# Kernel tuning notes

Hardware: AMD Instinct MI355X
Metric: run time of the kernel (lower is better)

The kernel has to match this reference:

```python
import jax, jax.numpy as jnp
import numpy as np

T = 4096
HID = 64          # hidden size (hard-coded 64 in forward)
EMB = 8           # direction embed size
NA = 7            # num actions
CONV_OUT = 64 * 15 * 15   # 64x64 input -> 31x31 -> 15x15, 64 channels
RIN = CONV_OUT + EMB      # GRU input size = 14408


def setup_inputs() -> dict:
    key = jax.random.key(0)
    ks = jax.random.split(key, 16)
    s = 0.05
    return {
        "image": jax.random.uniform(ks[0], (T, 1, 64, 64, 3), dtype=jnp.float32) * 255.0,
        "direction": jax.random.randint(ks[1], (T, 1), 0, 4),
        "conv1_w": jax.random.normal(ks[2], (32, 3, 3, 3), dtype=jnp.float32) * s,
        "conv1_b": jax.random.normal(ks[3], (32,), dtype=jnp.float32) * s,
        "conv2_w": jax.random.normal(ks[4], (64, 32, 3, 3), dtype=jnp.float32) * s,
        "conv2_b": jax.random.normal(ks[5], (64,), dtype=jnp.float32) * s,
        "emb": jax.random.normal(ks[6], (4, EMB), dtype=jnp.float32) * s,
        "w_ih": jax.random.normal(ks[7], (3 * HID, RIN), dtype=jnp.float32) * s,
        "b_ih": jax.random.normal(ks[8], (3 * HID,), dtype=jnp.float32) * s,
        "w_hh": jax.random.normal(ks[9], (3 * HID, HID), dtype=jnp.float32) * s,
        "b_hh": jax.random.normal(ks[10], (3 * HID,), dtype=jnp.float32) * s,
        "actor_w": jax.random.normal(ks[11], (NA, HID), dtype=jnp.float32) * s,
        "actor_b": jax.random.normal(ks[12], (NA,), dtype=jnp.float32) * s,
        "critic_w": jax.random.normal(ks[13], (1, HID), dtype=jnp.float32) * s,
        "critic_b": jax.random.normal(ks[14], (1,), dtype=jnp.float32) * s,
    }


def _conv(x, w, b):
    y = jax.lax.conv_general_dilated(x, w, (2, 2), 'VALID',
                                     dimension_numbers=('NCHW', 'OIHW', 'NCHW'))
    return jax.nn.relu(y + b[None, :, None, None])


def reference(image, direction, conv1_w, conv1_b, conv2_w, conv2_b, emb,
              w_ih, b_ih, w_hh, b_hh, actor_w, actor_b, critic_w, critic_b):
    img = image[:, 0]              # [T,H,W,3]  (squeeze env-batch dim)
    d = direction[:, 0]            # [T]
    x = (img / 255.0).transpose(0, 3, 1, 2)        # NCHW [T,3,64,64]
    x = _conv(x, conv1_w, conv1_b)                 # [T,32,31,31]
    x = _conv(x, conv2_w, conv2_b)                 # [T,64,15,15]
    conv_out = x.reshape(x.shape[0], -1)           # [T,14400] (C,H,W order == torch Flatten)
    feat = jnp.concatenate([conv_out, emb[d]], axis=1)   # [T,RIN]

    # Precompute input-side gate projections for all timesteps in one GEMM
    gx = feat @ w_ih.T + b_ih                      # [T,3H]

    def step(h, gx_t):
        gh = h @ w_hh.T + b_hh                     # [3H]
        r = jax.nn.sigmoid(gx_t[:HID] + gh[:HID])
        z = jax.nn.sigmoid(gx_t[HID:2*HID] + gh[HID:2*HID])
        n = jnp.tanh(gx_t[2*HID:] + r * gh[2*HID:])
        h_new = (1.0 - z) * n + z * h
        return h_new, h_new

    _, hs = jax.lax.scan(step, jnp.zeros((HID,), dtype=feat.dtype), gx)  # [T,HID]

    logits = hs @ actor_w.T + actor_b              # [T,NA]
    values = (hs @ critic_w.T + critic_b)[:, 0]    # [T]
    policy = jax.nn.softmax(logits, axis=-1)
    return policy, values
```

## Files before the change

kernel.cpp:

```cpp
#include <hip/hip_runtime.h>

#define T_STEPS 4096
#define HID 64
#define FEAT_LD 14464
#define SPLITK 8

typedef unsigned int uint;
typedef unsigned short ushort_t;
typedef _Float16 h2v __attribute__((ext_vector_type(2)));
typedef _Float16 v8h __attribute__((ext_vector_type(8)));
typedef float v4f __attribute__((ext_vector_type(4)));

__device__ __forceinline__ uint cvtpk(float a, float b) {
  return __builtin_bit_cast(uint, __builtin_amdgcn_cvt_pkrtz(a, b));
}
__device__ __forceinline__ uint packrelu(float a, float b) {
  return __builtin_bit_cast(
      uint, __builtin_amdgcn_cvt_pkrtz(fmaxf(a, 0.f), fmaxf(b, 0.f)));
}
__device__ __forceinline__ ushort_t hrelu(float a) {
  _Float16 h = (_Float16)fmaxf(a, 0.f);
  return __builtin_bit_cast(ushort_t, h);
}

__global__ __launch_bounds__(256) void prep_b(const float* __restrict__ w_ih,
                                              _Float16* __restrict__ Bw) {
  int i = blockIdx.x * 256 + threadIdx.x;
  if (i >= 192 * FEAT_LD) return;
  int row = i / FEAT_LD, col = i - row * FEAT_LD;
  float v = 0.f;
  if (col < 14400) {
    int p = col >> 6, oc = col & 63;
    v = w_ih[row * 14408 + oc * 225 + p];
  } else if (col < 14408) {
    v = w_ih[row * 14408 + col];
  }
  Bw[i] = (_Float16)v;
}

__global__ __launch_bounds__(256) void prep_conv(const float* __restrict__ w1,
                                                 const float* __restrict__ w2,
                                                 _Float16* __restrict__ bpack1,
                                                 _Float16* __restrict__ bpack) {
  int t = blockIdx.x * 256 + threadIdx.x;
  if (t < 2048) {
    int j = t & 7, l = (t >> 3) & 63, nf = (t >> 9) & 1, ks = t >> 10;
    int k = ks * 32 + ((l >> 4) * 8) + j;
    int cc = k & 3, kk = k >> 2;
    int oc = nf * 16 + (l & 15);
    float v = (cc < 3 && kk < 9) ? w1[oc * 27 + cc * 9 + kk] : 0.f;
    bpack1[t] = (_Float16)v;
  }
  if (t < 18432) {
    int j = t & 7, l = (t >> 3) & 63, nf = (t >> 9) & 3, kk = t >> 11;
    int oc = nf * 16 + (l & 15), ic = (l >> 4) * 8 + j;
    bpack[t] = (_Float16)w2[oc * 288 + ic * 9 + kk];
  }
}

__global__ __launch_bounds__(512, 4) void conv_kernel(
    const float* __restrict__ image, const int* __restrict__ dir,
    const _Float16* __restrict__ bpack1, const float* __restrict__ b1,
    const _Float16* __restrict__ bpack, const float* __restrict__ b2,
    const float* __restrict__ emb, _Float16* __restrict__ feat, int imgBase) {
  __shared__ __align__(16) _Float16 img_s[1216 * 4];
  __shared__ __align__(16) char c1_s[288 * 64];

  ushort_t* out_s = (ushort_t*)img_s;

  const int tid = threadIdx.x;
  const int wid = tid >> 6, lane = tid & 63;
  const int lrow = lane & 15, lq = lane >> 4;
  const int qh = blockIdx.x;
  const int img = imgBase + blockIdx.y;
  const int q3 = (qh == 3);
  const int nrows = q3 ? 16 : 19;
  const int nvalid = q3 ? 217 : 279;
  const int npos = q3 ? 45 : 60;
  const float* ip = image + (size_t)img * 12288 + (size_t)qh * 16 * 192;
  _Float16* fr = feat + (size_t)blockIdx.y * FEAT_LD;

  const int nf = wid & 3, mh = wid >> 2;
  v8h wb[9];
#pragma unroll
  for (int kk = 0; kk < 9; ++kk)
    wb[kk] = *(const v8h*)(bpack + ((size_t)(kk * 4 + nf) * 64 + lane) * 8);

  v8h bw1[2][2];
#pragma unroll
  for (int f = 0; f < 2; ++f)
#pragma unroll
    for (int ks = 0; ks < 2; ++ks)
      bw1[f][ks] =
          *(const v8h*)(bpack1 + ((size_t)(ks * 2 + f) * 64 + lane) * 8);
  const float4 b1q0 = *(const float4*)(b1 + lq * 4);
  const float4 b1q1 = *(const float4*)(b1 + 16 + lq * 4);

  const float kn = 1.f / 255.f;
  const int ng = nrows * 16;
  for (int g = tid; g < ng; g += 512) {
    const float* s0 = ip + g * 12;
    float4 A = *(const float4*)s0, B = *(const float4*)(s0 + 4),
           C = *(const float4*)(s0 + 8);
    uint4 u0, u1;
    u0.x = cvtpk(A.x * kn, A.y * kn);
    u0.y = cvtpk(A.z * kn, 0.f);
    u0.z = cvtpk(A.w * kn, B.x * kn);
    u0.w = cvtpk(B.y * kn, 0.f);
    u1.x = cvtpk(B.z * kn, B.w * kn);
    u1.y = cvtpk(C.x * kn, 0.f);
    u1.z = cvtpk(C.y * kn, C.z * kn);
    u1.w = cvtpk(C.w * kn, 0.f);
    *(uint4*)(img_s + g * 16) = u0;
    *(uint4*)(img_s + g * 16 + 8) = u1;
  }
  if (qh == 0 && tid < 64) {
    int d = dir[img];
    fr[14400 + tid] = (tid < 8) ? (_Float16)emb[d * 8 + tid] : (_Float16)0.f;
  }

  const int kk0 = 2 * lq, kk1 = 2 * lq + 1;
  const int off0 = ((kk0 / 3) * 64 + (kk0 - 3 * (kk0 / 3))) * 4;
  const int off1 = ((kk1 / 3) * 64 + (kk1 - 3 * (kk1 / 3))) * 4;
  const int off8 = (2 * 64 + 2) * 4;
  __syncthreads();

#pragma unroll
  for (int f = 0; f < 3; ++f) {
    const int mf = wid + 8 * f;
    if (mf >= 18) break;
    const int pin = mf * 16 + lrow;
    const int pv = (pin < 279) ? pin : 278;
    const int ly = pv / 31, lx = pv - 31 * ly;
    const _Float16* pb = img_s + ((2 * ly) * 64 + 2 * lx) * 4;
    uint2 p0 = *(const uint2*)(pb + off0);
    uint2 p1 = *(const uint2*)(pb + off1);
    uint2 p8 = *(const uint2*)(pb + off8);
    uint4 u0;
    u0.x = p0.x; u0.y = p0.y; u0.z = p1.x; u0.w = p1.y;
    uint4 u1;
    u1.x = (lq == 0) ? p8.x : 0u;
    u1.y = (lq == 0) ? p8.y : 0u;
    u1.z = 0u; u1.w = 0u;
    v8h a0 = __builtin_bit_cast(v8h, u0);
    v8h a1 = __builtin_bit_cast(v8h, u1);
    v4f ac0 = __builtin_bit_cast(v4f, b1q0);
    v4f ac1 = __builtin_bit_cast(v4f, b1q1);
    ac0 = __builtin_amdgcn_mfma_f32_16x16x32_f16(bw1[0][0], a0, ac0, 0, 0, 0);
    ac0 = __builtin_amdgcn_mfma_f32_16x16x32_f16(bw1[0][1], a1, ac0, 0, 0, 0);
    ac1 = __builtin_amdgcn_mfma_f32_16x16x32_f16(bw1[1][0], a0, ac1, 0, 0, 0);
    ac1 = __builtin_amdgcn_mfma_f32_16x16x32_f16(bw1[1][1], a1, ac1, 0, 0, 0);
    if (pin < nvalid) {
      char* base = c1_s + ((pin & 1) * 144 + (pin >> 1)) * 64;
      const int sw = (pin >> 2) & 3;
      uint2 u;
      u.x = packrelu(ac0[0], ac0[1]);
      u.y = packrelu(ac0[2], ac0[3]);
      *(uint2*)(base + ((((lq >> 1) ^ sw) << 4) + (lq & 1) * 8)) = u;
      u.x = packrelu(ac1[0], ac1[1]);
      u.y = packrelu(ac1[2], ac1[3]);
      *(uint2*)(base + ((((2 + (lq >> 1)) ^ sw) << 4) + (lq & 1) * 8)) = u;
    }
  }
  __syncthreads();

  int abase[2];
#pragma unroll
  for (int i = 0; i < 2; ++i) {
    int pos = (2 * mh + i) * 16 + lrow;
    int pv2 = (pos < npos) ? pos : 0;
    int oy = pv2 / 15, ox = pv2 - 15 * oy;
    abase[i] = (2 * oy) * 31 + 2 * ox;
  }
  v4f acc[2];
  {
    float bv = b2[nf * 16 + lrow];
    acc[0] = (v4f){bv, bv, bv, bv};
    acc[1] = acc[0];
  }
#pragma unroll
  for (int kk = 0; kk < 9; ++kk) {
    const int dd = (kk / 3) * 31 + (kk - 3 * (kk / 3));
#pragma unroll
    for (int i = 0; i < 2; ++i) {
      const int pin = abase[i] + dd;
      const int sw = (pin >> 2) & 3;
      const char* base = c1_s + ((pin & 1) * 144 + (pin >> 1)) * 64;
      v8h af = *(const v8h*)(base + ((lq ^ sw) << 4));
      acc[i] =
          __builtin_amdgcn_mfma_f32_16x16x32_f16(af, wb[kk], acc[i], 0, 0, 0);
    }
  }
  __syncthreads();
  {
#pragma unroll
    for (int i = 0; i < 2; ++i) {
      int oc = nf * 16 + lrow;
#pragma unroll
      for (int q = 0; q < 4; ++q) {
        int p = (2 * mh + i) * 16 + lq * 4 + q;
        out_s[p * 64 + (oc ^ ((p & 3) << 4))] = hrelu(acc[i][q]);
      }
    }
  }
  __syncthreads();
  {
    uint2* fr2 = (uint2*)fr + 16 * (60 * qh);
    const int nj = npos * 16;
    for (int j = tid; j < nj; j += 512) {
      int p = j >> 4, slot = j & 15;
      uint2 v = *(const uint2*)(out_s + p * 64 + ((slot << 2) ^ ((p & 3) << 4)));
      fr2[j] = v;
    }
  }
}

__global__ __launch_bounds__(256, 2) void gemm_kernel(
    const _Float16* __restrict__ feat, const _Float16* __restrict__ Bw,
    float* __restrict__ gxp, int rowBase, int mt) {
  __shared__ __align__(16) _Float16 As[2][64 * 64];
  __shared__ __align__(16) _Float16 Bs[2][192 * 64];
  const int tid = threadIdx.x;
  const int w = tid >> 6, lane = tid & 63;
  const int lrow = lane & 15, lq = lane >> 4;

  const int nwg = mt * SPLITK;
  const int q = nwg >> 3, r = nwg & 7;
  const int xcd = blockIdx.x & 7, pos = blockIdx.x >> 3;
  const int wg = (xcd < r ? xcd * (q + 1) : r * (q + 1) + (xcd - r) * q) + pos;
  const int sk = wg / mt, m = wg - sk * mt;
  const int bm = m * 64;
  const int ks0 = (sk * 226) / SPLITK, ks1 = ((sk + 1) * 226) / SPLITK;

  int rowA[2], kcA[2], offA[2], rowB[6], kcB[6], offB[6];
#pragma unroll
  for (int i = 0; i < 2; ++i) {
    int s = w * 128 + i * 64 + lane;
    rowA[i] = s >> 3;
    kcA[i] = s & 7;
    offA[i] = rowA[i] * 128 + ((kcA[i] ^ (rowA[i] & 7)) << 4);
  }
#pragma unroll
  for (int i = 0; i < 6; ++i) {
    int s = w * 384 + i * 64 + lane;
    rowB[i] = s >> 3;
    kcB[i] = s & 7;
    offB[i] = rowB[i] * 128 + ((kcB[i] ^ (rowB[i] & 7)) << 4);
  }

  uint4 ta[2], tb[6];
  {
    int kb = ks0 * 64;
#pragma unroll
    for (int i = 0; i < 2; ++i)
      ta[i] = *(const uint4*)(feat + (size_t)(bm + rowA[i]) * FEAT_LD + kb +
                              kcA[i] * 8);
#pragma unroll
    for (int i = 0; i < 6; ++i)
      tb[i] = *(const uint4*)(Bw + (size_t)rowB[i] * FEAT_LD + kb + kcB[i] * 8);
#pragma unroll
    for (int i = 0; i < 2; ++i) *(uint4*)((char*)As[0] + offA[i]) = ta[i];
#pragma unroll
    for (int i = 0; i < 6; ++i) *(uint4*)((char*)Bs[0] + offB[i]) = tb[i];
  }
  __syncthreads();

  v4f acc[4][3] = {};
  for (int ks = ks0; ks < ks1; ++ks) {
    const int cur = (ks - ks0) & 1;
    const bool more = (ks + 1 < ks1);
    if (more) {
      int kb = (ks + 1) * 64;
#pragma unroll
      for (int i = 0; i < 2; ++i)
        ta[i] = *(const uint4*)(feat + (size_t)(bm + rowA[i]) * FEAT_LD + kb +
                                kcA[i] * 8);
#pragma unroll
      for (int i = 0; i < 6; ++i)
        tb[i] =
            *(const uint4*)(Bw + (size_t)rowB[i] * FEAT_LD + kb + kcB[i] * 8);
    }
    const char* Ab = (const char*)As[cur];
    const char* Bb = (const char*)Bs[cur];
#pragma unroll
    for (int ksub = 0; ksub < 2; ++ksub) {
      int s0 = ksub * 4 + lq;
      v8h afr[4];
#pragma unroll
      for (int mf = 0; mf < 4; ++mf) {
        int row = mf * 16 + lrow;
        afr[mf] = *(const v8h*)(Ab + row * 128 + ((s0 ^ (row & 7)) << 4));
      }
#pragma unroll
      for (int nfi = 0; nfi < 3; ++nfi) {
        int col = (w * 3 + nfi) * 16 + lrow;
        v8h bfr = *(const v8h*)(Bb + col * 128 + ((s0 ^ (col & 7)) << 4));
#pragma unroll
        for (int mf = 0; mf < 4; ++mf)
          acc[mf][nfi] = __builtin_amdgcn_mfma_f32_16x16x32_f16(
              afr[mf], bfr, acc[mf][nfi], 0, 0, 0);
      }
    }
    if (more) {
      char* An = (char*)As[cur ^ 1];
      char* Bn = (char*)Bs[cur ^ 1];
#pragma unroll
      for (int i = 0; i < 2; ++i) *(uint4*)(An + offA[i]) = ta[i];
#pragma unroll
      for (int i = 0; i < 6; ++i) *(uint4*)(Bn + offB[i]) = tb[i];
    }
    __syncthreads();
  }
  const size_t obase = (size_t)sk * T_STEPS;
#pragma unroll
  for (int mf = 0; mf < 4; ++mf) {
#pragma unroll
    for (int nfi = 0; nfi < 3; ++nfi) {
      int col = (w * 3 + nfi) * 16 + lrow;
#pragma unroll
      for (int qq = 0; qq < 4; ++qq) {
        int rowm = bm + mf * 16 + lq * 4 + qq;
        gxp[(obase + rowBase + rowm) * 192 + col] = acc[mf][nfi][qq];
      }
    }
  }
}

__global__ __launch_bounds__(256) void reduce_gx(const float* __restrict__ gxp,
                                                 const float* __restrict__ b_ih,
                                                 float* __restrict__ gx) {
  int t = blockIdx.x * 256 + threadIdx.x;
  if (t >= T_STEPS * 192) return;
  int col = t - (t / 192) * 192;
  float s = b_ih[col];
#pragma unroll
  for (int k = 0; k < SPLITK; ++k) s += gxp[(size_t)k * T_STEPS * 192 + t];
  gx[t] = s;
}

__global__ __launch_bounds__(192) void scan_kernel(
    const float* __restrict__ gx, const float* __restrict__ w_hh,
    const float* __restrict__ b_hh, float* __restrict__ hs, int C, int W) {
  __shared__ __align__(16) float h_s[64];
  __shared__ float r_s[64], z_s[64];
  const int tid = threadIdx.x;
  const int g = tid >> 6, j = tid & 63;
  const int b = blockIdx.x;
  const int tstore = b * C;
  const int t0 = max(0, tstore - W);
  const int t1 = tstore + C;

  float w[64];
#pragma unroll
  for (int k4 = 0; k4 < 16; ++k4) {
    float4 v = *(const float4*)(w_hh + tid * 64 + k4 * 4);
    w[4 * k4 + 0] = v.x;
    w[4 * k4 + 1] = v.y;
    w[4 * k4 + 2] = v.z;
    w[4 * k4 + 3] = v.w;
  }
  const float bh = b_hh[tid];
  if (tid < 64) h_s[tid] = 0.f;
  __syncthreads();

  float gxv = gx[(size_t)t0 * 192 + tid];
  for (int t = t0; t < t1; ++t) {
    int tn = (t + 1 < T_STEPS) ? t + 1 : T_STEPS - 1;
    float gxn = gx[(size_t)tn * 192 + tid];
    float gacc0 = bh, gacc1 = 0.f, gacc2 = 0.f, gacc3 = 0.f;
#pragma unroll
    for (int k4 = 0; k4 < 4; ++k4) {
      float4 hA = *(const float4*)(h_s + 0 + k4 * 4);
      float4 hB = *(const float4*)(h_s + 16 + k4 * 4);
      float4 hC = *(const float4*)(h_s + 32 + k4 * 4);
      float4 hD = *(const float4*)(h_s + 48 + k4 * 4);
      gacc0 = fmaf(w[0 + 4 * k4], hA.x, gacc0);
      gacc0 = fmaf(w[1 + 4 * k4], hA.y, gacc0);
      gacc0 = fmaf(w[2 + 4 * k4], hA.z, gacc0);
      gacc0 = fmaf(w[3 + 4 * k4], hA.w, gacc0);
      gacc1 = fmaf(w[16 + 4 * k4], hB.x, gacc1);
      gacc1 = fmaf(w[17 + 4 * k4], hB.y, gacc1);
      gacc1 = fmaf(w[18 + 4 * k4], hB.z, gacc1);
      gacc1 = fmaf(w[19 + 4 * k4], hB.w, gacc1);
      gacc2 = fmaf(w[32 + 4 * k4], hC.x, gacc2);
      gacc2 = fmaf(w[33 + 4 * k4], hC.y, gacc2);
      gacc2 = fmaf(w[34 + 4 * k4], hC.z, gacc2);
      gacc2 = fmaf(w[35 + 4 * k4], hC.w, gacc2);
      gacc3 = fmaf(w[48 + 4 * k4], hD.x, gacc3);
      gacc3 = fmaf(w[49 + 4 * k4], hD.y, gacc3);
      gacc3 = fmaf(w[50 + 4 * k4], hD.z, gacc3);
      gacc3 = fmaf(w[51 + 4 * k4], hD.w, gacc3);
    }
    float gh = (gacc0 + gacc1) + (gacc2 + gacc3);
    if (g == 0)
      r_s[j] = 1.f / (1.f + __expf(-(gxv + gh)));
    else if (g == 1)
      z_s[j] = 1.f / (1.f + __expf(-(gxv + gh)));
    __syncthreads();
    if (g == 2) {
      float r = r_s[j], z = z_s[j];
      float x = gxv + r * gh;
      float x2 = fminf(fmaxf(2.f * x, -30.f), 30.f);
      float e = __expf(x2);
      float n = (e - 1.f) / (e + 1.f);
      float hn = (1.f - z) * n + z * h_s[j];
      h_s[j] = hn;
      if (t >= tstore) hs[(size_t)t * 64 + j] = hn;
    }
    __syncthreads();
    gxv = gxn;
  }
}

__global__ __launch_bounds__(256) void head_kernel(
    const float* __restrict__ hs, const float* __restrict__ aw,
    const float* __restrict__ ab, const float* __restrict__ cw,
    const float* __restrict__ cb, float* __restrict__ out) {
  int t = blockIdx.x * 256 + threadIdx.x;
  if (t >= T_STEPS) return;
  float h[64];
#pragma unroll
  for (int i = 0; i < 16; ++i) {
    float4 v = *(const float4*)(hs + (size_t)t * 64 + 4 * i);
    h[4 * i + 0] = v.x;
    h[4 * i + 1] = v.y;
    h[4 * i + 2] = v.z;
    h[4 * i + 3] = v.w;
  }
  float lg[7];
#pragma unroll
  for (int o = 0; o < 7; ++o) {
    float a = ab[o];
#pragma unroll
    for (int jj = 0; jj < 64; ++jj) a = fmaf(aw[o * 64 + jj], h[jj], a);
    lg[o] = a;
  }
  float v = cb[0];
#pragma unroll
  for (int jj = 0; jj < 64; ++jj) v = fmaf(cw[jj], h[jj], v);
  float m = lg[0];
#pragma unroll
  for (int o = 1; o < 7; ++o) m = fmaxf(m, lg[o]);
  float e[7], s = 0.f;
#pragma unroll
  for (int o = 0; o < 7; ++o) {
    e[o] = __expf(lg[o] - m);
    s += e[o];
  }
  float inv = 1.f / s;
#pragma unroll
  for (int o = 0; o < 7; ++o) out[(size_t)t * 7 + o] = e[o] * inv;
  out[(size_t)T_STEPS * 7 + t] = v;
}

extern "C" void kernel_launch(void* const* d_in, const int* in_sizes, int n_in,
                              void* d_out, int out_size, void* d_ws,
                              size_t ws_size, hipStream_t stream) {
  const float* image = (const float*)d_in[0];
  const int* dir = (const int*)d_in[1];
  const float* w1 = (const float*)d_in[2];
  const float* b1 = (const float*)d_in[3];
  const float* w2 = (const float*)d_in[4];
  const float* b2 = (const float*)d_in[5];
  const float* emb = (const float*)d_in[6];
  const float* w_ih = (const float*)d_in[7];
  const float* b_ih = (const float*)d_in[8];
  const float* w_hh = (const float*)d_in[9];
  const float* b_hh = (const float*)d_in[10];
  const float* aw = (const float*)d_in[11];
  const float* ab = (const float*)d_in[12];
  const float* cw = (const float*)d_in[13];
  const float* cb = (const float*)d_in[14];
  float* out = (float*)d_out;

  const size_t bp1Bytes = 4096;
  const size_t bpackBytes = 18432 * 2;
  const size_t bBytes = (size_t)192 * FEAT_LD * 2;
  const size_t gxpBytes = (size_t)SPLITK * T_STEPS * 192 * 4;
  const size_t gxBytes = (size_t)T_STEPS * 192 * 4;
  const size_t hsBytes = (size_t)T_STEPS * 64 * 4;
  const size_t fixed =
      bp1Bytes + bpackBytes + bBytes + gxpBytes + gxBytes + hsBytes;
  int CH = 4096;
  while (CH > 256 && fixed + (size_t)CH * FEAT_LD * 2 > ws_size) CH >>= 1;

  char* p = (char*)d_ws;
  _Float16* bpack1 = (_Float16*)p;
  p += bp1Bytes;
  _Float16* bpack = (_Float16*)p;
  p += bpackBytes;
  _Float16* Bw = (_Float16*)p;
  p += bBytes;
  float* gxp = (float*)p;
  p += gxpBytes;
  float* gx = (float*)p;
  p += gxBytes;
  float* hs = (float*)p;
  p += hsBytes;
  _Float16* featBuf = (_Float16*)p;

  prep_conv<<<72, 256, 0, stream>>>(w1, w2, bpack1, bpack);
  prep_b<<<(192 * FEAT_LD + 255) / 256, 256, 0, stream>>>(w_ih, Bw);
  for (int c = 0; c < T_STEPS; c += CH) {
    conv_kernel<<<dim3(4, CH), 512, 0, stream>>>(image, dir, bpack1, b1, bpack,
                                                 b2, emb, featBuf, c);
    gemm_kernel<<<(CH / 64) * SPLITK, 256, 0, stream>>>(featBuf, Bw, gxp, c,
                                                        CH / 64);
  }
  reduce_gx<<<(T_STEPS * 192 + 255) / 256, 256, 0, stream>>>(gxp, b_ih, gx);
  scan_kernel<<<512, 192, 0, stream>>>(gx, w_hh, b_hh, hs, 8, 152);
  head_kernel<<<(T_STEPS + 255) / 256, 256, 0, stream>>>(hs, aw, ab, cw, cb,
                                                         out);
}
```

Baseline: 413.3 us.

## Process whole image per conv block with double-buffered quarter staging

```diff
diff --git a/kernel.cpp b/kernel.cpp
--- a/kernel.cpp
+++ b/kernel.cpp
@@ -63,28 +63,27 @@
     const _Float16* __restrict__ bpack1, const float* __restrict__ b1,
     const _Float16* __restrict__ bpack, const float* __restrict__ b2,
     const float* __restrict__ emb, _Float16* __restrict__ feat, int imgBase) {
-  __shared__ __align__(16) _Float16 img_s[1216 * 4];
+  __shared__ __align__(16) _Float16 img_c[2][1216 * 4];
   __shared__ __align__(16) char c1_s[288 * 64];
-
-  ushort_t* out_s = (ushort_t*)img_s;
+  __shared__ __align__(16) ushort_t out_s[64 * 64];
 
   const int tid = threadIdx.x;
   const int wid = tid >> 6, lane = tid & 63;
   const int lrow = lane & 15, lq = lane >> 4;
-  const int qh = blockIdx.x;
-  const int img = imgBase + blockIdx.y;
-  const int q3 = (qh == 3);
-  const int nrows = q3 ? 16 : 19;
-  const int nvalid = q3 ? 217 : 279;
-  const int npos = q3 ? 45 : 60;
-  const float* ip = image + (size_t)img * 12288 + (size_t)qh * 16 * 192;
-  _Float16* fr = feat + (size_t)blockIdx.y * FEAT_LD;
+  const int img = imgBase + blockIdx.x;
+  const float* ip = image + (size_t)img * 12288;
+  _Float16* fr = feat + (size_t)blockIdx.x * FEAT_LD;
+  const float kn = 1.f / 255.f;
 
   const int nf = wid & 3, mh = wid >> 2;
   v8h wb[9];
 #pragma unroll
-  for (int kk = 0; kk < 9; ++kk)
-    wb[kk] = *(const v8h*)(bpack + ((size_t)(kk * 4 + nf) * 64 + lane) * 8);
+  for (int kk = 0; kk < 9; ++kk) {
+    uint4 t = *(const uint4*)(bpack + ((size_t)(kk * 4 + nf) * 64 + lane) * 8);
+    asm volatile("" : "+v"(t.x), "+v"(t.y), "+v"(t.z), "+v"(t.w));
+    wb[kk] = __builtin_bit_cast(v8h, t);
+  }
+  const float b2v = b2[nf * 16 + lrow];
 
   v8h bw1[2][2];
 #pragma unroll
@@ -96,10 +95,18 @@
   const float4 b1q0 = *(const float4*)(b1 + lq * 4);
   const float4 b1q1 = *(const float4*)(b1 + 16 + lq * 4);
 
-  const float kn = 1.f / 255.f;
-  const int ng = nrows * 16;
-  for (int g = tid; g < ng; g += 512) {
-    const float* s0 = ip + g * 12;
+  const int kk0 = 2 * lq, kk1 = 2 * lq + 1;
+  const int off0 = ((kk0 / 3) * 64 + (kk0 - 3 * (kk0 / 3))) * 4;
+  const int off1 = ((kk1 / 3) * 64 + (kk1 - 3 * (kk1 / 3))) * 4;
+  const int off8 = (2 * 64 + 2) * 4;
+
+  if (tid < 64) {
+    int d = dir[img];
+    fr[14400 + tid] = (tid < 8) ? (_Float16)emb[d * 8 + tid] : (_Float16)0.f;
+  }
+
+  if (tid < 304) {
+    const float* s0 = ip + tid * 12;
     float4 A = *(const float4*)s0, B = *(const float4*)(s0 + 4),
            C = *(const float4*)(s0 + 8);
     uint4 u0, u1;
@@ -111,107 +118,126 @@
     u1.y = cvtpk(C.x * kn, 0.f);
     u1.z = cvtpk(C.y * kn, C.z * kn);
     u1.w = cvtpk(C.w * kn, 0.f);
-    *(uint4*)(img_s + g * 16) = u0;
-    *(uint4*)(img_s + g * 16 + 8) = u1;
-  }
-  if (qh == 0 && tid < 64) {
-    int d = dir[img];
-    fr[14400 + tid] = (tid < 8) ? (_Float16)emb[d * 8 + tid] : (_Float16)0.f;
-  }
-
-  const int kk0 = 2 * lq, kk1 = 2 * lq + 1;
-  const int off0 = ((kk0 / 3) * 64 + (kk0 - 3 * (kk0 / 3))) * 4;
-  const int off1 = ((kk1 / 3) * 64 + (kk1 - 3 * (kk1 / 3))) * 4;
-  const int off8 = (2 * 64 + 2) * 4;
+    *(uint4*)(img_c[0] + tid * 16) = u0;
+    *(uint4*)(img_c[0] + tid * 16 + 8) = u1;
+  }
   __syncthreads();
 
-#pragma unroll
-  for (int f = 0; f < 3; ++f) {
-    const int mf = wid + 8 * f;
-    if (mf >= 18) break;
-    const int pin = mf * 16 + lrow;
-    const int pv = (pin < 279) ? pin : 278;
-    const int ly = pv / 31, lx = pv - 31 * ly;
-    const _Float16* pb = img_s + ((2 * ly) * 64 + 2 * lx) * 4;
-    uint2 p0 = *(const uint2*)(pb + off0);
-    uint2 p1 = *(const uint2*)(pb + off1);
-    uint2 p8 = *(const uint2*)(pb + off8);
-    uint4 u0;
-    u0.x = p0.x; u0.y = p0.y; u0.z = p1.x; u0.w = p1.y;
-    uint4 u1;
-    u1.x = (lq == 0) ? p8.x : 0u;
-    u1.y = (lq == 0) ? p8.y : 0u;
-    u1.z = 0u; u1.w = 0u;
-    v8h a0 = __builtin_bit_cast(v8h, u0);
-    v8h a1 = __builtin_bit_cast(v8h, u1);
-    v4f ac0 = __builtin_bit_cast(v4f, b1q0);
-    v4f ac1 = __builtin_bit_cast(v4f, b1q1);
-    ac0 = __builtin_amdgcn_mfma_f32_16x16x32_f16(bw1[0][0], a0, ac0, 0, 0, 0);
-    ac0 = __builtin_amdgcn_mfma_f32_16x16x32_f16(bw1[0][1], a1, ac0, 0, 0, 0);
-    ac1 = __builtin_amdgcn_mfma_f32_16x16x32_f16(bw1[1][0], a0, ac1, 0, 0, 0);
-    ac1 = __builtin_amdgcn_mfma_f32_16x16x32_f16(bw1[1][1], a1, ac1, 0, 0, 0);
-    if (pin < nvalid) {
-      char* base = c1_s + ((pin & 1) * 144 + (pin >> 1)) * 64;
-      const int sw = (pin >> 2) & 3;
-      uint2 u;
-      u.x = packrelu(ac0[0], ac0[1]);
-      u.y = packrelu(ac0[2], ac0[3]);
-      *(uint2*)(base + ((((lq >> 1) ^ sw) << 4) + (lq & 1) * 8)) = u;
-      u.x = packrelu(ac1[0], ac1[1]);
-      u.y = packrelu(ac1[2], ac1[3]);
-      *(uint2*)(base + ((((2 + (lq >> 1)) ^ sw) << 4) + (lq & 1) * 8)) = u;
-    }
-  }
-  __syncthreads();
-
-  int abase[2];
-#pragma unroll
-  for (int i = 0; i < 2; ++i) {
-    int pos = (2 * mh + i) * 16 + lrow;
-    int pv2 = (pos < npos) ? pos : 0;
-    int oy = pv2 / 15, ox = pv2 - 15 * oy;
-    abase[i] = (2 * oy) * 31 + 2 * ox;
-  }
-  v4f acc[2];
-  {
-    float bv = b2[nf * 16 + lrow];
-    acc[0] = (v4f){bv, bv, bv, bv};
+  int buf = 0;
+  for (int q = 0; q < 4; ++q) {
+    const int q3 = (q == 3);
+    const int nvalid = q3 ? 217 : 279;
+    const int npos = q3 ? 45 : 60;
+    float4 La, Lb, Lc;
+    const int ngn = (q + 1 < 3) ? 304 : 256;
+    const bool doStage = (q < 3) && (tid < ngn);
+    if (doStage) {
+      const float* sn = ip + (size_t)(16 * (q + 1)) * 192 + tid * 12;
+      La = *(const float4*)sn;
+      Lb = *(const float4*)(sn + 4);
+      Lc = *(const float4*)(sn + 8);
+    }
+
+#pragma unroll
+    for (int f = 0; f < 3; ++f) {
+      const int mf = wid + 8 * f;
+      if (mf >= 18) break;
+      const int pin = mf * 16 + lrow;
+      const int pv = (pin < 279) ? pin : 278;
+      const int ly = pv / 31, lx = pv - 31 * ly;
+      const _Float16* pb = img_c[buf] + ((2 * ly) * 64 + 2 * lx) * 4;
+      uint2 p0 = *(const uint2*)(pb + off0);
+      uint2 p1 = *(const uint2*)(pb + off1);
+      uint2 p8 = *(const uint2*)(pb + off8);
+      uint4 u0;
+      u0.x = p0.x; u0.y = p0.y; u0.z = p1.x; u0.w = p1.y;
+      uint4 u1;
+      u1.x = (lq == 0) ? p8.x : 0u;
+      u1.y = (lq == 0) ? p8.y : 0u;
+      u1.z = 0u; u1.w = 0u;
+      v8h a0 = __builtin_bit_cast(v8h, u0);
+      v8h a1 = __builtin_bit_cast(v8h, u1);
+      v4f ac0 = __builtin_bit_cast(v4f, b1q0);
+      v4f ac1 = __builtin_bit_cast(v4f, b1q1);
+      ac0 = __builtin_amdgcn_mfma_f32_16x16x32_f16(bw1[0][0], a0, ac0, 0, 0, 0);
+      ac0 = __builtin_amdgcn_mfma_f32_16x16x32_f16(bw1[0][1], a1, ac0, 0, 0, 0);
+      ac1 = __builtin_amdgcn_mfma_f32_16x16x32_f16(bw1[1][0], a0, ac1, 0, 0, 0);
+      ac1 = __builtin_amdgcn_mfma_f32_16x16x32_f16(bw1[1][1], a1, ac1, 0, 0, 0);
+      if (pin < nvalid) {
+        char* base = c1_s + ((pin & 1) * 144 + (pin >> 1)) * 64;
+        const int sw = (pin >> 2) & 3;
+        uint2 u;
+        u.x = packrelu(ac0[0], ac0[1]);
+        u.y = packrelu(ac0[2], ac0[3]);
+        *(uint2*)(base + ((((lq >> 1) ^ sw) << 4) + (lq & 1) * 8)) = u;
+        u.x = packrelu(ac1[0], ac1[1]);
+        u.y = packrelu(ac1[2], ac1[3]);
+        *(uint2*)(base + ((((2 + (lq >> 1)) ^ sw) << 4) + (lq & 1) * 8)) = u;
+      }
+    }
+    __syncthreads();
+
+    if (doStage) {
+      _Float16* dst = img_c[buf ^ 1];
+      uint4 u0, u1;
+      u0.x = cvtpk(La.x * kn, La.y * kn);
+      u0.y = cvtpk(La.z * kn, 0.f);
+      u0.z = cvtpk(La.w * kn, Lb.x * kn);
+      u0.w = cvtpk(Lb.y * kn, 0.f);
+      u1.x = cvtpk(Lb.z * kn, Lb.w * kn);
+      u1.y = cvtpk(Lc.x * kn, 0.f);
+      u1.z = cvtpk(Lc.y * kn, Lc.z * kn);
+      u1.w = cvtpk(Lc.w * kn, 0.f);
+      *(uint4*)(dst + tid * 16) = u0;
+      *(uint4*)(dst + tid * 16 + 8) = u1;
+    }
+
+    int abase[2];
+#pragma unroll
+    for (int i = 0; i < 2; ++i) {
+      int pos = (2 * mh + i) * 16 + lrow;
+      int pv2 = (pos < npos) ? pos : 0;
+      int oy = pv2 / 15, ox = pv2 - 15 * oy;
+      abase[i] = (2 * oy) * 31 + 2 * ox;
+    }
+    v4f acc[2];
+    acc[0] = (v4f){b2v, b2v, b2v, b2v};
     acc[1] = acc[0];
-  }
-#pragma unroll
-  for (int kk = 0; kk < 9; ++kk) {
-    const int dd = (kk / 3) * 31 + (kk - 3 * (kk / 3));
-#pragma unroll
-    for (int i = 0; i < 2; ++i) {
-      const int pin = abase[i] + dd;
-      const int sw = (pin >> 2) & 3;
-      const char* base = c1_s + ((pin & 1) * 144 + (pin >> 1)) * 64;
-      v8h af = *(const v8h*)(base + ((lq ^ sw) << 4));
-      acc[i] =
-          __builtin_amdgcn_mfma_f32_16x16x32_f16(af, wb[kk], acc[i], 0, 0, 0);
-    }
-  }
-  __syncthreads();
-  {
+#pragma unroll
+    for (int kk = 0; kk < 9; ++kk) {
+      const int dd = (kk / 3) * 31 + (kk - 3 * (kk / 3));
+#pragma unroll
+      for (int i = 0; i < 2; ++i) {
+        const int pin = abase[i] + dd;
+        const int sw = (pin >> 2) & 3;
+        const char* base = c1_s + ((pin & 1) * 144 + (pin >> 1)) * 64;
+        v8h af = *(const v8h*)(base + ((lq ^ sw) << 4));
+        acc[i] =
+            __builtin_amdgcn_mfma_f32_16x16x32_f16(af, wb[kk], acc[i], 0, 0, 0);
+      }
+    }
 #pragma unroll
     for (int i = 0; i < 2; ++i) {
       int oc = nf * 16 + lrow;
 #pragma unroll
-      for (int q = 0; q < 4; ++q) {
-        int p = (2 * mh + i) * 16 + lq * 4 + q;
-        out_s[p * 64 + (oc ^ ((p & 3) << 4))] = hrelu(acc[i][q]);
-      }
-    }
-  }
-  __syncthreads();
-  {
-    uint2* fr2 = (uint2*)fr + 16 * (60 * qh);
-    const int nj = npos * 16;
-    for (int j = tid; j < nj; j += 512) {
-      int p = j >> 4, slot = j & 15;
-      uint2 v = *(const uint2*)(out_s + p * 64 + ((slot << 2) ^ ((p & 3) << 4)));
-      fr2[j] = v;
-    }
+      for (int qq = 0; qq < 4; ++qq) {
+        int p = (2 * mh + i) * 16 + lq * 4 + qq;
+        out_s[p * 64 + (oc ^ ((p & 3) << 4))] = hrelu(acc[i][qq]);
+      }
+    }
+    __syncthreads();
+
+    {
+      uint2* fr2 = (uint2*)fr + 16 * (60 * q);
+      const int nj = npos * 16;
+      for (int j = tid; j < nj; j += 512) {
+        int p = j >> 4, slot = j & 15;
+        uint2 v =
+            *(const uint2*)(out_s + p * 64 + ((slot << 2) ^ ((p & 3) << 4)));
+        fr2[j] = v;
+      }
+    }
+    buf ^= 1;
   }
 }
 
@@ -502,8 +528,8 @@
   prep_conv<<<72, 256, 0, stream>>>(w1, w2, bpack1, bpack);
   prep_b<<<(192 * FEAT_LD + 255) / 256, 256, 0, stream>>>(w_ih, Bw);
   for (int c = 0; c < T_STEPS; c += CH) {
-    conv_kernel<<<dim3(4, CH), 512, 0, stream>>>(image, dir, bpack1, b1, bpack,
-                                                 b2, emb, featBuf, c);
+    conv_kernel<<<CH, 512, 0, stream>>>(image, dir, bpack1, b1, bpack, b2, emb,
+                                        featBuf, c);
     gemm_kernel<<<(CH / 64) * SPLITK, 256, 0, stream>>>(featBuf, Bw, gxp, c,
                                                         CH / 64);
   }
```

After: 470.1 us. +13.7%, slower.
